# Performance work log

Hardware: AMD Instinct MI355X
Metric: run time of the kernel (lower is better)

## Reference

```python
import jax, jax.numpy as jnp
from jax import lax
import numpy as np

B, C, H, W = 16, 32, 128, 128
R = 8      # region_num
OUT = 32   # out_channels (== in_channels, required by residual add)
K = 3      # kernel_size
PAD = 1    # self.kwargs padding for the correlation conv


def setup_inputs() -> dict:
    key = jax.random.key(0)
    ks = jax.random.split(key, 8)
    n = lambda k, s: jax.random.normal(k, s, dtype=jnp.float32) * 0.05
    return {
        "input": jax.random.normal(ks[0], (B, C, H, W), dtype=jnp.float32),
        "guide_input": jax.random.normal(ks[1], (B, C, H, W), dtype=jnp.float32),
        "w1": n(ks[2], (R * R, C)), "b1": jnp.zeros((R * R,), jnp.float32),
        "w2": n(ks[3], (R, C * OUT, R)), "b2": jnp.zeros((R * C * OUT,), jnp.float32),
        "w_spa": n(ks[4], (R, C)), "b_spa": jnp.zeros((R,), jnp.float32),
        "w_spec": n(ks[5], (R, C)), "b_spec": jnp.zeros((R,), jnp.float32),
        "w_f": n(ks[6], (OUT, 2 * C, 3, 3)), "b_f": jnp.zeros((OUT,), jnp.float32),
    }


def adaptive_avg_pool2d(x, k):
    # torch AdaptiveAvgPool2d bin edges: start=floor(i*H/k), end=ceil((i+1)*H/k)
    Hh, Ww = x.shape[-2], x.shape[-1]
    rows = []
    for i in range(k):
        hs, he = (i * Hh) // k, -(-((i + 1) * Hh) // k)
        cols = []
        for j in range(k):
            ws, we = (j * Ww) // k, -(-((j + 1) * Ww) // k)
            cols.append(x[..., hs:he, ws:we].mean(axis=(-2, -1)))
        rows.append(jnp.stack(cols, axis=-1))
    return jnp.stack(rows, axis=-2)  # [..., k, k]


def asign_index(kernel, guide):
    # kernel: [B, R, OUT, H, W]; guide: [B, R, H, W]
    mask = jax.nn.one_hot(jnp.argmax(guide, axis=1), guide.shape[1], axis=1,
                          dtype=kernel.dtype)  # [B, R, H, W]
    return jnp.sum(kernel * mask[:, :, None], axis=1)  # [B, OUT, H, W]


def reference(input, guide_input, w1, b1, w2, b2, w_spa, b_spa, w_spec, b_spec, w_f, b_f):
    # --- dynamic kernel generation (conv_kernel Sequential) ---
    pooled = adaptive_avg_pool2d(input, K)                                    # [B, C, K, K]
    g = jax.nn.sigmoid(jnp.einsum('bckl,oc->bokl', pooled, w1) + b1[None, :, None, None])  # [B, R*R, K, K]
    g = g.reshape(B, R, R, K, K)
    # grouped 1x1 conv (groups=R): per group in=R, out=C*OUT
    kern = jnp.einsum('brikl,roi->brokl', g, w2).reshape(B, R * C * OUT, K, K)
    kern = kern + b2[None, :, None, None]
    kern = kern.reshape(B, R * OUT, C, K, K)

    # --- correlation: per-sample conv with its own generated kernels (xcorr_fast) ---
    corr = jax.vmap(lambda xi, ki: lax.conv_general_dilated(
        xi[None], ki, (1, 1), [(PAD, PAD), (PAD, PAD)])[0])(input, kern)      # [B, R*OUT, H, W]
    corr = corr.reshape(B, R, OUT, H, W)

    # --- guide features (SpecDynConv / SpecClassifier modeled as 1x1 convs C->R) ---
    gf_spa = jnp.einsum('bchw,rc->brhw', guide_input, w_spa) + b_spa[None, :, None, None]
    gf_spec = jnp.einsum('bchw,rc->brhw', guide_input, w_spec) + b_spec[None, :, None, None]

    # --- argmax one-hot mask select + region-sum ---
    out_spa = asign_index(corr, gf_spa)    # [B, OUT, H, W]
    out_spec = asign_index(corr, gf_spec)  # [B, OUT, H, W]

    # --- fusion conv 3x3 + residual ---
    fused = lax.conv_general_dilated(jnp.concatenate([out_spa, out_spec], axis=1),
                                     w_f, (1, 1), [(1, 1), (1, 1)])
    fused = fused + b_f[None, :, None, None]
    return fused + input
```

## Files before the change

kernel.cpp:

```cpp
#include <hip/hip_runtime.h>
#include <hip/hip_bf16.h>
#include <math.h>

#define Bn 16
#define Cn 32
#define Hn 128
#define Wn 128
#define HW (Hn*Wn)
#define Rn 8
#define OUTn 32
#define PW 130

#define OFF_POOLED 0u
#define OFF_G      18432u
#define OFF_KERNA  55296u
#define OFF_WFA    2414592u
#define OFF_RSEL   2451456u
#define OFF_INTP   3500032u
#define OFF_CATP   20805632u

typedef __attribute__((ext_vector_type(8))) short short8;
typedef __attribute__((ext_vector_type(4))) float floatx4;

static __device__ __forceinline__ unsigned short f2b(float f) {
  __hip_bfloat16 h = __float2bfloat16(f);
  return *reinterpret_cast<unsigned short*>(&h);
}


__global__ void g_kernel(const float* __restrict__ poolsum, const float* __restrict__ w1,
                         const float* __restrict__ b1, float* __restrict__ g) {
  const int idx = blockIdx.x * 256 + threadIdx.x;
  if (idx >= Bn * 64 * 9) return;
  const int bin = idx % 9;
  const int o = (idx / 9) % 64;
  const int b = idx / (9 * 64);
  const int bi = bin / 3, bj = bin % 3;
  const float szr[3] = {43.f, 44.f, 43.f};
  const float invn = 1.f / (szr[bi] * szr[bj]);
  float acc = b1[o];
  #pragma unroll
  for (int c = 0; c < Cn; ++c)
    acc = fmaf(poolsum[(b * Cn + c) * 9 + bin] * invn, w1[o * Cn + c], acc);
  g[idx] = 1.f / (1.f + expf(-acc));
}

__global__ void kern_kernel(const float* __restrict__ g, const float* __restrict__ w2,
                            const float* __restrict__ b2, short* __restrict__ kernA) {
  const int idx = blockIdx.x * 256 + threadIdx.x;
  if (idx >= Bn * 8 * 9 * 1024) return;
  const int j  = idx & 7;
  const int m  = (idx >> 3) & 15;
  const int kg = (idx >> 7) & 3;
  const int h  = (idx >> 9) & 1;
  const int t  = (idx >> 10) % 9;
  const int br = idx / 9216;
  const int r = br & 7, b = br >> 3;
  const int c = kg * 8 + j;
  const int u = h * 16 + m;
  const int jidx = u * 32 + c;
  float acc = b2[r * 1024 + jidx];
  #pragma unroll
  for (int i = 0; i < 8; ++i)
    acc = fmaf(g[(b * 64 + r * 8 + i) * 9 + t], w2[(r * 1024 + jidx) * 8 + i], acc);
  kernA[idx] = (short)f2b(acc);
}

__global__ void wf_kernel(const float* __restrict__ w_f, short* __restrict__ wfA) {
  int idx = blockIdx.x * 256 + threadIdx.x;
  if (idx >= 18432) return;
  const int j  = idx & 7;
  const int m  = (idx >> 3) & 15;
  const int kg = (idx >> 7) & 3;
  const int h  = (idx >> 9) & 1;
  const int kb = idx >> 10;
  const int tap = kb >> 1, ch = kb & 1;
  const int ci = ch * 32 + kg * 8 + j;
  const int o = h * 16 + m;
  wfA[idx] = (short)f2b(w_f[(o * 64 + ci) * 9 + tap]);
}


__global__ void halo_kernel(uint4* __restrict__ inTp, uint4* __restrict__ catp,
                            float* __restrict__ poolsum) {
  const int idx = blockIdx.x * 256 + threadIdx.x;
  if (idx < Bn * Cn * 9) poolsum[idx] = 0.f;
  if (idx >= Bn * 520) return;
  const int b = idx / 520, i = idx % 520;
  int y, x;
  if (i < 130)      { y = 0;       x = i; }
  else if (i < 260) { y = 129;     x = i - 130; }
  else if (i < 390) { y = i - 260; x = 0; }
  else              { y = i - 390; x = 129; }
  const size_t pp = (size_t)(b * PW + y) * PW + x;
  const uint4 z = make_uint4(0u, 0u, 0u, 0u);
  #pragma unroll
  for (int q = 0; q < 4; ++q) inTp[pp * 4 + q] = z;
  #pragma unroll
  for (int q = 0; q < 8; ++q) catp[pp * 8 + q] = z;
}


__global__ __launch_bounds__(256) void tr_kernel(const float* __restrict__ in,
                                                 uint4* __restrict__ inTp,
                                                 float* __restrict__ poolsum) {
  __shared__ float lds[32][65];
  const int blk = blockIdx.x;
  const int b = blk >> 8;
  const int p0 = (blk & 255) * 64;
  const int tid = threadIdx.x;
  const int pl = tid & 63;
  const int c0 = tid >> 6;
  #pragma unroll
  for (int cc = 0; cc < 8; ++cc) {
    const int c = cc * 4 + c0;
    lds[c][pl] = in[(size_t)(b * 32 + c) * HW + p0 + pl];
  }
  __syncthreads();
  {
    const int pw = tid >> 2;
    const int cg = (tid & 3) * 8;
    unsigned int w0 = (unsigned)f2b(lds[cg + 0][pw]) | ((unsigned)f2b(lds[cg + 1][pw]) << 16);
    unsigned int w1 = (unsigned)f2b(lds[cg + 2][pw]) | ((unsigned)f2b(lds[cg + 3][pw]) << 16);
    unsigned int w2 = (unsigned)f2b(lds[cg + 4][pw]) | ((unsigned)f2b(lds[cg + 5][pw]) << 16);
    unsigned int w3 = (unsigned)f2b(lds[cg + 6][pw]) | ((unsigned)f2b(lds[cg + 7][pw]) << 16);
    const int p = p0 + pw;
    const int y = p >> 7, x = p & 127;
    const size_t pp = (size_t)(b * PW + y + 1) * PW + (x + 1);
    inTp[pp * 4 + (tid & 3)] = make_uint4(w0, w1, w2, w3);
  }
  const int x0 = p0 & 127;
  const int y  = p0 >> 7;
  const int c  = tid >> 3, j = tid & 7;
  const int plo = j * 8;
  const int splitA = x0 ? 22 : 43;
  const int splitB = x0 ? 21 : 42;
  float sumA = 0.f, sumB = 0.f;
  #pragma unroll
  for (int k = 0; k < 8; ++k) {
    const float v = lds[c][plo + k];
    if (plo + k < splitA)  sumA += v;
    if (plo + k >= splitB) sumB += v;
  }
  sumA += __shfl_down(sumA, 4, 64); sumB += __shfl_down(sumB, 4, 64);
  sumA += __shfl_down(sumA, 2, 64); sumB += __shfl_down(sumB, 2, 64);
  sumA += __shfl_down(sumA, 1, 64); sumB += __shfl_down(sumB, 1, 64);
  if (j == 0) {
    const int bi0 = (y < 43) ? 0 : ((y < 86) ? 1 : 2);
    const int bi1 = (y == 42) ? 1 : ((y == 85) ? 2 : -1);
    const int bjA = x0 ? 1 : 0, bjB = x0 ? 2 : 1;
    float* ps = poolsum + (b * Cn + c) * 9;
    atomicAdd(ps + bi0 * 3 + bjA, sumA);
    atomicAdd(ps + bi0 * 3 + bjB, sumB);
    if (bi1 >= 0) {
      atomicAdd(ps + bi1 * 3 + bjA, sumA);
      atomicAdd(ps + bi1 * 3 + bjB, sumB);
    }
  }
}


__global__ void rsel_kernel(const float* __restrict__ guide,
                            const float* __restrict__ w_spa, const float* __restrict__ b_spa,
                            const float* __restrict__ w_spec, const float* __restrict__ b_spec,
                            int* __restrict__ rsel) {
  const int idx = blockIdx.x * 256 + threadIdx.x;
  const int b = idx >> 14;
  const int p = idx & (HW - 1);
  float gv[Cn];
  const float* gp = guide + (size_t)b * Cn * HW + p;
  #pragma unroll
  for (int c = 0; c < Cn; ++c) gv[c] = gp[c * HW];
  int best1 = 0, best2 = 0;
  float bv1 = -1e30f, bv2 = -1e30f;
  for (int r = 0; r < Rn; ++r) {
    float v1 = b_spa[r], v2 = b_spec[r];
    #pragma unroll
    for (int c = 0; c < Cn; ++c) {
      v1 = fmaf(gv[c], w_spa[r * Cn + c], v1);
      v2 = fmaf(gv[c], w_spec[r * Cn + c], v2);
    }
    if (v1 > bv1) { bv1 = v1; best1 = r; }
    if (v2 > bv2) { bv2 = v2; best2 = r; }
  }
  rsel[idx] = best1 | (best2 << 8);
}


__global__ void stageB_kernel(
    const char* __restrict__ inTp, const short* __restrict__ kernA,
    const int* __restrict__ rsel, char* __restrict__ catp) {
  const int id = blockIdx.x;
  const int chunk = id & 7, r = (id >> 3) & 7, b = id >> 6;
  const int pbase = chunk * 2048;
  __shared__ int lcount;
  __shared__ unsigned short list[4096];
  const int tid = threadIdx.x;
  if (tid == 0) lcount = 0;
  __syncthreads();
  const int* rs = rsel + b * HW + pbase;
  for (int i = tid; i < 2048; i += 256) {
    int v = rs[i];
    if ((v & 255) == r) { int k = atomicAdd(&lcount, 1); list[k] = (unsigned short)i; }
    if ((v >> 8) == r)  { int k = atomicAdd(&lcount, 1); list[k] = (unsigned short)(i | 2048); }
  }
  __syncthreads();
  const int cnt = lcount;
  const int lane = tid & 63, wid = tid >> 6;
  const int l15 = lane & 15, kg = lane >> 4;

  short8 aw[18];
  {
    const short* kb = kernA + (size_t)(b * 8 + r) * 18 * 512;
    #pragma unroll
    for (int f = 0; f < 18; ++f)
      aw[f] = *(const short8*)(kb + f * 512 + kg * 128 + l15 * 8);
  }

  for (int g = wid; g * 16 < cnt; g += 4) {
    const int e16 = g * 16 + l15;
    const bool ev = e16 < cnt;
    const int ent = list[ev ? e16 : 0];
    const int p = pbase + (ent & 2047);
    const int which = ent >> 11;
    const int y = p >> 7, x = p & 127;
    const size_t pp = (size_t)(b * PW + y + 1) * PW + (x + 1);
    const char* base = inTp + pp * 64 + kg * 16;
    short8 bx[9];
    #pragma unroll
    for (int t = 0; t < 9; ++t) {
      const int dy = t / 3 - 1, dx = t % 3 - 1;
      bx[t] = *(const short8*)(base + (dy * PW + dx) * 64);
    }
    floatx4 acc0 = {0.f, 0.f, 0.f, 0.f}, acc1 = {0.f, 0.f, 0.f, 0.f};
    #pragma unroll
    for (int t = 0; t < 9; ++t) {
      acc0 = __builtin_amdgcn_mfma_f32_16x16x32_bf16(aw[t * 2 + 0], bx[t], acc0, 0, 0, 0);
      acc1 = __builtin_amdgcn_mfma_f32_16x16x32_bf16(aw[t * 2 + 1], bx[t], acc1, 0, 0, 0);
    }
    if (ev) {
      char* op = catp + pp * 128 + which * 64 + kg * 8;
      uint2 v0, v1;
      v0.x = (unsigned)f2b(acc0[0]) | ((unsigned)f2b(acc0[1]) << 16);
      v0.y = (unsigned)f2b(acc0[2]) | ((unsigned)f2b(acc0[3]) << 16);
      v1.x = (unsigned)f2b(acc1[0]) | ((unsigned)f2b(acc1[1]) << 16);
      v1.y = (unsigned)f2b(acc1[2]) | ((unsigned)f2b(acc1[3]) << 16);
      *(uint2*)op = v0;
      *(uint2*)(op + 32) = v1;
    }
  }
}


__global__ __launch_bounds__(256, 4) void stageC_kernel(
    const char* __restrict__ catp, const short* __restrict__ wfA,
    const float* __restrict__ b_f, const float* __restrict__ in,
    float* __restrict__ out) {
  __shared__ short lwf[18432];
  const int tid = threadIdx.x;
  {
    const uint4* src = (const uint4*)wfA;
    uint4* dst = (uint4*)lwf;
    #pragma unroll
    for (int i = 0; i < 9; ++i)
      dst[i * 256 + tid] = src[i * 256 + tid];
  }
  __syncthreads();
  const int id = (blockIdx.x & 7) * 128 + (blockIdx.x >> 3);
  const int b = id >> 6, seg = id & 63;
  const int lane = tid & 63, wid = tid >> 6;
  const int l15 = lane & 15, kg = lane >> 4;
  const int pix = seg * 256 + wid * 64 + l15;

  const char* bq[4];
  #pragma unroll
  for (int q = 0; q < 4; ++q) {
    const int p = pix + q * 16;
    const int y = p >> 7, x = p & 127;
    bq[q] = catp + ((size_t)(b * PW + y + 1) * PW + (x + 1)) * 128 + kg * 16;
  }
  floatx4 acc[2][4] = {};
  short8 bxA[8], bxB[8];

#define GOFF(T) (((((T) / 3) - 1) * PW + (((T) % 3) - 1)) * 128)

#define LOADTAP(BUF, T)                                              \
  { _Pragma("unroll")                                                \
    for (int q = 0; q < 4; ++q) {                                    \
      BUF[q * 2 + 0] = *(const short8*)(bq[q] + GOFF(T));            \
      BUF[q * 2 + 1] = *(const short8*)(bq[q] + GOFF(T) + 64);       \
    } }

#define MFMATAP(BUF, T)                                                              \
  { const short8 a00 = *(const short8*)&lwf[(4*(T)+0)*512 + kg*128 + l15*8];          \
    const short8 a01 = *(const short8*)&lwf[(4*(T)+1)*512 + kg*128 + l15*8];          \
    const short8 a10 = *(const short8*)&lwf[(4*(T)+2)*512 + kg*128 + l15*8];          \
    const short8 a11 = *(const short8*)&lwf[(4*(T)+3)*512 + kg*128 + l15*8];          \
    _Pragma("unroll")                                                                 \
    for (int q = 0; q < 4; ++q) {                                                     \
      acc[0][q] = __builtin_amdgcn_mfma_f32_16x16x32_bf16(a00, BUF[q*2+0], acc[0][q], 0, 0, 0); \
      acc[1][q] = __builtin_amdgcn_mfma_f32_16x16x32_bf16(a01, BUF[q*2+0], acc[1][q], 0, 0, 0); \
      acc[0][q] = __builtin_amdgcn_mfma_f32_16x16x32_bf16(a10, BUF[q*2+1], acc[0][q], 0, 0, 0); \
      acc[1][q] = __builtin_amdgcn_mfma_f32_16x16x32_bf16(a11, BUF[q*2+1], acc[1][q], 0, 0, 0); \
    } }

  LOADTAP(bxA, 0)
  LOADTAP(bxB, 1)  MFMATAP(bxA, 0)
  LOADTAP(bxA, 2)  MFMATAP(bxB, 1)
  LOADTAP(bxB, 3)  MFMATAP(bxA, 2)
  LOADTAP(bxA, 4)  MFMATAP(bxB, 3)
  LOADTAP(bxB, 5)  MFMATAP(bxA, 4)
  LOADTAP(bxA, 6)  MFMATAP(bxB, 5)
  LOADTAP(bxB, 7)  MFMATAP(bxA, 6)
  LOADTAP(bxA, 8)  MFMATAP(bxB, 7)
                   MFMATAP(bxA, 8)
#undef LOADTAP
#undef MFMATAP
#undef GOFF

  #pragma unroll
  for (int h = 0; h < 2; ++h) {
    const int o0 = h * 16 + kg * 4;
    #pragma unroll
    for (int q = 0; q < 4; ++q) {
      const int p = pix + q * 16;
      #pragma unroll
      for (int reg = 0; reg < 4; ++reg) {
        const size_t oi = (size_t)(b * 32 + o0 + reg) * HW + p;
        out[oi] = acc[h][q][reg] + b_f[o0 + reg] + in[oi];
      }
    }
  }
}


extern "C" void kernel_launch(void* const* d_in, const int* in_sizes, int n_in,
                              void* d_out, int out_size, void* d_ws, size_t ws_size,
                              hipStream_t stream) {
  const float* input  = (const float*)d_in[0];
  const float* guide  = (const float*)d_in[1];
  const float* w1     = (const float*)d_in[2];
  const float* b1     = (const float*)d_in[3];
  const float* w2     = (const float*)d_in[4];
  const float* b2     = (const float*)d_in[5];
  const float* w_spa  = (const float*)d_in[6];
  const float* b_spa  = (const float*)d_in[7];
  const float* w_spec = (const float*)d_in[8];
  const float* b_spec = (const float*)d_in[9];
  const float* w_f    = (const float*)d_in[10];
  const float* b_f    = (const float*)d_in[11];
  float* out = (float*)d_out;

  char* ws = (char*)d_ws;
  float* poolsum = (float*)(ws + OFF_POOLED);
  float* g      = (float*)(ws + OFF_G);
  short* kernA  = (short*)(ws + OFF_KERNA);
  short* wfA    = (short*)(ws + OFF_WFA);
  int*   rsel   = (int*)(ws + OFF_RSEL);
  uint4* inTp   = (uint4*)(ws + OFF_INTP);
  char*  catp   = (char*)(ws + OFF_CATP);

  wf_kernel<<<72, 256, 0, stream>>>(w_f, wfA);
  halo_kernel<<<(Bn * 520 + 255) / 256, 256, 0, stream>>>(inTp, (uint4*)catp, poolsum);
  tr_kernel<<<Bn * 256, 256, 0, stream>>>(input, inTp, poolsum);
  g_kernel<<<(Bn * 64 * 9 + 255) / 256, 256, 0, stream>>>(poolsum, w1, b1, g);
  kern_kernel<<<Bn * 8 * 9 * 1024 / 256, 256, 0, stream>>>(g, w2, b2, kernA);
  rsel_kernel<<<Bn * HW / 256, 256, 0, stream>>>(guide, w_spa, b_spa, w_spec, b_spec, rsel);
  stageB_kernel<<<1024, 256, 0, stream>>>((const char*)inTp, kernA, rsel, catp);
  stageC_kernel<<<1024, 256, 0, stream>>>(catp, wfA, b_f, input, out);
}
```

Before: 265.3 us.

## Fold halo zeroing into other kernels, stage guide via LDS, deepen stageC pipeline

The halo-zeroing kernel is removed: poolsum clearing moves into wf_kernel and halo border zeroing moves into rsel_kernel, which saves one launch. rsel_kernel now stages the guide tile through shared memory before computing. stageB interleaves each tap load with its MFMAs so fewer registers are live at once. stageC moves to a three-buffer load pipeline with launch bounds relaxed to 3 waves, trading occupancy for deeper memory prefetch.

After: 264.0 us. About the same (-0.5%).

```diff
diff --git a/kernel.cpp b/kernel.cpp
--- a/kernel.cpp
+++ b/kernel.cpp
@@ -66,8 +66,10 @@
   kernA[idx] = (short)f2b(acc);
 }
 
-__global__ void wf_kernel(const float* __restrict__ w_f, short* __restrict__ wfA) {
+__global__ void wf_kernel(const float* __restrict__ w_f, short* __restrict__ wfA,
+                          float* __restrict__ poolsum) {
   int idx = blockIdx.x * 256 + threadIdx.x;
+  if (idx < Bn * Cn * 9) poolsum[idx] = 0.f;
   if (idx >= 18432) return;
   const int j  = idx & 7;
   const int m  = (idx >> 3) & 15;
@@ -78,26 +80,6 @@
   const int ci = ch * 32 + kg * 8 + j;
   const int o = h * 16 + m;
   wfA[idx] = (short)f2b(w_f[(o * 64 + ci) * 9 + tap]);
-}
-
-
-__global__ void halo_kernel(uint4* __restrict__ inTp, uint4* __restrict__ catp,
-                            float* __restrict__ poolsum) {
-  const int idx = blockIdx.x * 256 + threadIdx.x;
-  if (idx < Bn * Cn * 9) poolsum[idx] = 0.f;
-  if (idx >= Bn * 520) return;
-  const int b = idx / 520, i = idx % 520;
-  int y, x;
-  if (i < 130)      { y = 0;       x = i; }
-  else if (i < 260) { y = 129;     x = i - 130; }
-  else if (i < 390) { y = i - 260; x = 0; }
-  else              { y = i - 390; x = 129; }
-  const size_t pp = (size_t)(b * PW + y) * PW + x;
-  const uint4 z = make_uint4(0u, 0u, 0u, 0u);
-  #pragma unroll
-  for (int q = 0; q < 4; ++q) inTp[pp * 4 + q] = z;
-  #pragma unroll
-  for (int q = 0; q < 8; ++q) catp[pp * 8 + q] = z;
 }
 
 
@@ -160,17 +142,40 @@
 }
 
 
-__global__ void rsel_kernel(const float* __restrict__ guide,
-                            const float* __restrict__ w_spa, const float* __restrict__ b_spa,
-                            const float* __restrict__ w_spec, const float* __restrict__ b_spec,
-                            int* __restrict__ rsel) {
-  const int idx = blockIdx.x * 256 + threadIdx.x;
-  const int b = idx >> 14;
-  const int p = idx & (HW - 1);
+__global__ __launch_bounds__(256) void rsel_kernel(
+    const float* __restrict__ guide,
+    const float* __restrict__ w_spa, const float* __restrict__ b_spa,
+    const float* __restrict__ w_spec, const float* __restrict__ b_spec,
+    int* __restrict__ rsel, uint4* __restrict__ inTp, uint4* __restrict__ catp) {
+  const int tid = threadIdx.x;
+  {
+    const int hidx = blockIdx.x * 256 + tid;
+    if (hidx < Bn * 520) {
+      const int hb = hidx / 520, i = hidx % 520;
+      int y, x;
+      if (i < 130)      { y = 0;       x = i; }
+      else if (i < 260) { y = 129;     x = i - 130; }
+      else if (i < 390) { y = i - 260; x = 0; }
+      else              { y = i - 390; x = 129; }
+      const size_t pp = (size_t)(hb * PW + y) * PW + x;
+      const uint4 z = make_uint4(0u, 0u, 0u, 0u);
+      #pragma unroll
+      for (int q = 0; q < 4; ++q) inTp[pp * 4 + q] = z;
+      #pragma unroll
+      for (int q = 0; q < 8; ++q) catp[pp * 8 + q] = z;
+    }
+  }
+  __shared__ float lds[32][256];
+  const int b = blockIdx.x >> 6;
+  const int p0 = (blockIdx.x & 63) * 256;
+  const float* gp = guide + (size_t)b * Cn * HW + p0;
+  #pragma unroll
+  for (int c = 0; c < Cn; ++c)
+    lds[c][tid] = gp[(size_t)c * HW + tid];
+  __syncthreads();
   float gv[Cn];
-  const float* gp = guide + (size_t)b * Cn * HW + p;
-  #pragma unroll
-  for (int c = 0; c < Cn; ++c) gv[c] = gp[c * HW];
+  #pragma unroll
+  for (int c = 0; c < Cn; ++c) gv[c] = lds[c][tid];
   int best1 = 0, best2 = 0;
   float bv1 = -1e30f, bv2 = -1e30f;
   for (int r = 0; r < Rn; ++r) {
@@ -183,11 +188,11 @@
     if (v1 > bv1) { bv1 = v1; best1 = r; }
     if (v2 > bv2) { bv2 = v2; best2 = r; }
   }
-  rsel[idx] = best1 | (best2 << 8);
-}
-
-
-__global__ void stageB_kernel(
+  rsel[b * HW + p0 + tid] = best1 | (best2 << 8);
+}
+
+
+__global__ __launch_bounds__(256) void stageB_kernel(
     const char* __restrict__ inTp, const short* __restrict__ kernA,
     const int* __restrict__ rsel, char* __restrict__ catp) {
   const int id = blockIdx.x;
@@ -226,17 +231,13 @@
     const int y = p >> 7, x = p & 127;
     const size_t pp = (size_t)(b * PW + y + 1) * PW + (x + 1);
     const char* base = inTp + pp * 64 + kg * 16;
-    short8 bx[9];
+    floatx4 acc0 = {0.f, 0.f, 0.f, 0.f}, acc1 = {0.f, 0.f, 0.f, 0.f};
     #pragma unroll
     for (int t = 0; t < 9; ++t) {
       const int dy = t / 3 - 1, dx = t % 3 - 1;
-      bx[t] = *(const short8*)(base + (dy * PW + dx) * 64);
-    }
-    floatx4 acc0 = {0.f, 0.f, 0.f, 0.f}, acc1 = {0.f, 0.f, 0.f, 0.f};
-    #pragma unroll
-    for (int t = 0; t < 9; ++t) {
-      acc0 = __builtin_amdgcn_mfma_f32_16x16x32_bf16(aw[t * 2 + 0], bx[t], acc0, 0, 0, 0);
-      acc1 = __builtin_amdgcn_mfma_f32_16x16x32_bf16(aw[t * 2 + 1], bx[t], acc1, 0, 0, 0);
+      const short8 bx = *(const short8*)(base + (dy * PW + dx) * 64);
+      acc0 = __builtin_amdgcn_mfma_f32_16x16x32_bf16(aw[t * 2 + 0], bx, acc0, 0, 0, 0);
+      acc1 = __builtin_amdgcn_mfma_f32_16x16x32_bf16(aw[t * 2 + 1], bx, acc1, 0, 0, 0);
     }
     if (ev) {
       char* op = catp + pp * 128 + which * 64 + kg * 8;
@@ -252,7 +253,7 @@
 }
 
 
-__global__ __launch_bounds__(256, 4) void stageC_kernel(
+__global__ __launch_bounds__(256, 3) void stageC_kernel(
     const char* __restrict__ catp, const short* __restrict__ wfA,
     const float* __restrict__ b_f, const float* __restrict__ in,
     float* __restrict__ out) {
@@ -280,7 +281,7 @@
     bq[q] = catp + ((size_t)(b * PW + y + 1) * PW + (x + 1)) * 128 + kg * 16;
   }
   floatx4 acc[2][4] = {};
-  short8 bxA[8], bxB[8];
+  short8 bxA[8], bxB[8], bxC[8];
 
 #define GOFF(T) (((((T) / 3) - 1) * PW + (((T) % 3) - 1)) * 128)
 
@@ -305,15 +306,17 @@
     } }
 
   LOADTAP(bxA, 0)
-  LOADTAP(bxB, 1)  MFMATAP(bxA, 0)
-  LOADTAP(bxA, 2)  MFMATAP(bxB, 1)
-  LOADTAP(bxB, 3)  MFMATAP(bxA, 2)
-  LOADTAP(bxA, 4)  MFMATAP(bxB, 3)
-  LOADTAP(bxB, 5)  MFMATAP(bxA, 4)
-  LOADTAP(bxA, 6)  MFMATAP(bxB, 5)
-  LOADTAP(bxB, 7)  MFMATAP(bxA, 6)
-  LOADTAP(bxA, 8)  MFMATAP(bxB, 7)
-                   MFMATAP(bxA, 8)
+  LOADTAP(bxB, 1)
+  LOADTAP(bxC, 2)
+  MFMATAP(bxA, 0)  LOADTAP(bxA, 3)
+  MFMATAP(bxB, 1)  LOADTAP(bxB, 4)
+  MFMATAP(bxC, 2)  LOADTAP(bxC, 5)
+  MFMATAP(bxA, 3)  LOADTAP(bxA, 6)
+  MFMATAP(bxB, 4)  LOADTAP(bxB, 7)
+  MFMATAP(bxC, 5)  LOADTAP(bxC, 8)
+  MFMATAP(bxA, 6)
+  MFMATAP(bxB, 7)
+  MFMATAP(bxC, 8)
 #undef LOADTAP
 #undef MFMATAP
 #undef GOFF
@@ -360,12 +363,12 @@
   uint4* inTp   = (uint4*)(ws + OFF_INTP);
   char*  catp   = (char*)(ws + OFF_CATP);
 
-  wf_kernel<<<72, 256, 0, stream>>>(w_f, wfA);
-  halo_kernel<<<(Bn * 520 + 255) / 256, 256, 0, stream>>>(inTp, (uint4*)catp, poolsum);
+  wf_kernel<<<72, 256, 0, stream>>>(w_f, wfA, poolsum);
   tr_kernel<<<Bn * 256, 256, 0, stream>>>(input, inTp, poolsum);
   g_kernel<<<(Bn * 64 * 9 + 255) / 256, 256, 0, stream>>>(poolsum, w1, b1, g);
   kern_kernel<<<Bn * 8 * 9 * 1024 / 256, 256, 0, stream>>>(g, w2, b2, kernA);
-  rsel_kernel<<<Bn * HW / 256, 256, 0, stream>>>(guide, w_spa, b_spa, w_spec, b_spec, rsel);
+  rsel_kernel<<<Bn * HW / 256, 256, 0, stream>>>(guide, w_spa, b_spa, w_spec, b_spec,
+                                                 rsel, inTp, (uint4*)catp);
   stageB_kernel<<<1024, 256, 0, stream>>>((const char*)inTp, kernA, rsel, catp);
   stageC_kernel<<<1024, 256, 0, stream>>>(catp, wfA, b_f, input, out);
 }
```
